# Kernel tuning notes

Measured on AMD Instinct MI355X. Metric: run time of the kernel, lower is better.

Reference implementation:

```python
import jax, jax.numpy as jnp
import numpy as np

N = 50000
HID = 128
NH = 4
E_RES, E_SEQ, E_KNN = 100000, 100000, 200000
BN_EPS = 1e-5
NEG_SLOPE = 0.2


def _gat(h, src, dst, W, al, ar, resW, b):
    """DGL-style GATConv (eval mode: feat_drop off, residual=True, bias).
    h: (N, in), W/resW: (in, H*out), al/ar: (H, out), b: (H*out,)"""
    Hh, out = al.shape
    feat = (h @ W).reshape(N, Hh, out)                 # (N, H, out)
    el = jnp.sum(feat * al, axis=-1)                   # (N, H)
    er = jnp.sum(feat * ar, axis=-1)                   # (N, H)
    e = jax.nn.leaky_relu(el[src] + er[dst], NEG_SLOPE)  # (E, H)
    # edge softmax over incoming edges of each dst node (numerically stable)
    m = jax.ops.segment_max(e, dst, num_segments=N)    # (N, H)
    ex = jnp.exp(e - m[dst])
    s = jax.ops.segment_sum(ex, dst, num_segments=N)
    a = ex / s[dst]                                    # (E, H)
    msg = a[:, :, None] * feat[src]                    # (E, H, out)
    rst = jax.ops.segment_sum(msg, dst, num_segments=N)  # (N, H, out)
    return rst + (h @ resW).reshape(N, Hh, out) + b.reshape(1, Hh, out)


def _hetero(h, src_res, dst_res, src_seq, dst_seq, src_knn, dst_knn, W, al, ar, resW, b):
    # HeteroGraphConv with aggregate='sum' over relations, then mean over heads
    r = _gat(h, src_res, dst_res, W[0], al[0], ar[0], resW[0], b[0])
    r = r + _gat(h, src_seq, dst_seq, W[1], al[1], ar[1], resW[1], b[1])
    r = r + _gat(h, src_knn, dst_knn, W[2], al[2], ar[2], resW[2], b[2])
    return jnp.mean(r, axis=1)                         # (N, out)


def setup_inputs() -> dict:
    key = jax.random.key(0)
    ks = iter(jax.random.split(key, 32))
    inp = {}
    inp["x"] = jax.random.normal(next(ks), (N, HID), jnp.float32)
    inp["src_res"] = jax.random.randint(next(ks), (E_RES,), 0, N, jnp.int32)
    inp["dst_res"] = jax.random.randint(next(ks), (E_RES,), 0, N, jnp.int32)
    inp["src_seq"] = jax.random.randint(next(ks), (E_SEQ,), 0, N, jnp.int32)
    inp["dst_seq"] = jax.random.randint(next(ks), (E_SEQ,), 0, N, jnp.int32)
    inp["src_knn"] = jax.random.randint(next(ks), (E_KNN,), 0, N, jnp.int32)
    inp["dst_knn"] = jax.random.randint(next(ks), (E_KNN,), 0, N, jnp.int32)
    sc = 0.05
    for l in (0, 1):
        inp[f"W{l}"] = jax.random.normal(next(ks), (3, HID, NH * HID), jnp.float32) * sc
        inp[f"al{l}"] = jax.random.normal(next(ks), (3, NH, HID), jnp.float32) * sc
        inp[f"ar{l}"] = jax.random.normal(next(ks), (3, NH, HID), jnp.float32) * sc
        inp[f"resW{l}"] = jax.random.normal(next(ks), (3, HID, NH * HID), jnp.float32) * sc
        inp[f"b{l}"] = jax.random.normal(next(ks), (3, NH * HID), jnp.float32) * sc
    inp["fc_W"] = jax.random.normal(next(ks), (HID, HID), jnp.float32) * sc
    inp["fc_b"] = jax.random.normal(next(ks), (HID,), jnp.float32) * sc
    inp["bn_gamma"] = jnp.ones((HID,), jnp.float32)
    inp["bn_beta"] = jnp.zeros((HID,), jnp.float32)
    inp["bn_mean"] = jax.random.normal(next(ks), (HID,), jnp.float32) * sc
    inp["bn_var"] = jax.random.uniform(next(ks), (HID,), jnp.float32)
    return inp


def reference(x, src_res, dst_res, src_seq, dst_seq, src_knn, dst_knn,
              W0, al0, ar0, resW0, b0, W1, al1, ar1, resW1, b1,
              fc_W, fc_b, bn_gamma, bn_beta, bn_mean, bn_var):
    # layer 0: hetero GAT, head-mean, fc + ReLU + BatchNorm (eval), dropout=identity
    h = _hetero(x, src_res, dst_res, src_seq, dst_seq, src_knn, dst_knn,
                W0, al0, ar0, resW0, b0)
    h = jax.nn.relu(h @ fc_W + fc_b)
    h = (h - bn_mean) / jnp.sqrt(bn_var + BN_EPS) * bn_gamma + bn_beta
    # layer 1 (final): hetero GAT, head-mean
    out = _hetero(h, src_res, dst_res, src_seq, dst_seq, src_knn, dst_knn,
                  W1, al1, ar1, resW1, b1)
    return out
```

## Files before the change

### kernel.cpp

```cpp
#include <hip/hip_runtime.h>
#include <hip/hip_bf16.h>
#include <math.h>
#include <stdint.h>

#define NNODES 50000
#define SCHUNK 4096
#define AW 1664
#define XOFF 1536

typedef __bf16 bf16x8 __attribute__((ext_vector_type(8)));
typedef float f32x4 __attribute__((ext_vector_type(4)));
typedef unsigned short u16;
typedef unsigned int u32;

__device__ __forceinline__ float lrelu(float x){ return x >= 0.f ? x : 0.2f*x; }
__device__ __forceinline__ float b2f(u16 u){ union{ u32 i; float f; } c; c.i = ((u32)u)<<16; return c.f; }
__device__ __forceinline__ float lo2f(u32 v){ union{ u32 i; float f; } c; c.i = v<<16; return c.f; }
__device__ __forceinline__ float hi2f(u32 v){ union{ u32 i; float f; } c; c.i = v & 0xffff0000u; return c.f; }
__device__ __forceinline__ u16 f2b(float f){ __hip_bfloat16 h = __float2bfloat16(f); return *(u16*)&h; }
__device__ __forceinline__ u32 packbf(float a, float b){ return (u32)f2b(a) | ((u32)f2b(b) << 16); }

__global__ void prep_b(const float* __restrict__ W0, const float* __restrict__ W1,
                       const float* __restrict__ resW0, const float* __restrict__ resW1,
                       const float* __restrict__ b0, const float* __restrict__ b1,
                       u16* __restrict__ Btb, float* __restrict__ biasf)
{
    int gid = blockIdx.x*blockDim.x + threadIdx.x;
    if (gid < 2*128*AW){
        int l = gid / (128*AW);
        int rem = gid - l*(128*AW);
        int c = rem / AW;
        int j = rem - c*AW;
        const float* W  = l ? W1 : W0;
        const float* rw = l ? resW1 : resW0;
        float v;
        if (j < XOFF){
            int r = j >> 9, h = (j >> 7) & 3, k = j & 127;
            v = 0.25f * W[(size_t)r*65536 + (size_t)k*512 + h*128 + c];
        } else {
            int k = j - XOFF;
            float s = 0.f;
            for (int r = 0; r < 3; ++r)
                for (int h = 0; h < 4; ++h)
                    s += rw[(size_t)r*65536 + (size_t)k*512 + h*128 + c];
            v = 0.25f * s;
        }
        Btb[gid] = f2b(v);
    }
    if (gid < 256){
        int l = gid >> 7, c = gid & 127;
        const float* bb = l ? b1 : b0;
        float s = 0.f;
        for (int r = 0; r < 3; ++r)
            for (int h = 0; h < 4; ++h)
                s += bb[r*512 + h*128 + c];
        biasf[gid] = 0.25f*s;
    }
}

__global__ void prep_wl(const float* __restrict__ W0, const float* __restrict__ W1,
                        const float* __restrict__ al0, const float* __restrict__ ar0,
                        const float* __restrict__ al1, const float* __restrict__ ar1,
                        const float* __restrict__ fcW,
                        u16* __restrict__ wlb, u16* __restrict__ fcWtb)
{
    int gid = blockIdx.x*blockDim.x + threadIdx.x;
    if (gid < 2*128*128){
        int l = gid >> 14;
        int col = (gid >> 7) & 127;
        int k = gid & 127;
        float v = 0.f;
        if (col < 24){
            int r = col >> 3, lr = (col >> 2) & 1, h = col & 3;
            const float* W = l ? W1 : W0;
            const float* av = l ? (lr ? ar1 : al1) : (lr ? ar0 : al0);
            const float* wrow = W + (size_t)r*65536 + (size_t)k*512 + h*128;
            const float* arow = av + r*512 + h*128;
            for (int cc = 0; cc < 128; ++cc) v += wrow[cc]*arow[cc];
        }
        wlb[gid] = f2b(v);
    }
    if (gid < 128*128){
        int k = gid & 127, n = gid >> 7;
        fcWtb[gid] = f2b(fcW[k*128 + n]);
    }
}

__global__ __launch_bounds__(256) void xprep_kernel(const float* __restrict__ x,
    u16* __restrict__ Ax, const u16* __restrict__ wl, float* __restrict__ el, int M)
{
    __shared__ u16 Xs[64*136];
    __shared__ u16 Ws[32*136];
    const int tid = threadIdx.x;
    const int row0 = blockIdx.x*64;
    #pragma unroll
    for (int p = 0; p < 2; ++p){
        int idx = tid + p*256;
        int c = idx >> 4, kc = (idx & 15)*8;
        float4 v = make_float4(0.f,0.f,0.f,0.f);
        if (c < 24) v = *(const float4*)(wl + c*128 + kc);
        *(float4*)&Ws[c*136 + kc] = v;
    }
    int r = tid >> 2, cq = (tid & 3)*32;
    int grow = row0 + r;
    if (grow < M){
        #pragma unroll
        for (int i = 0; i < 8; ++i){
            float4 v = *(const float4*)(x + (size_t)grow*128 + cq + i*4);
            ushort4 o;
            o.x = f2b(v.x); o.y = f2b(v.y); o.z = f2b(v.z); o.w = f2b(v.w);
            *(ushort4*)(Ax + (size_t)grow*AW + cq + i*4) = o;
            *(ushort4*)&Xs[r*136 + cq + i*4] = o;
        }
    } else {
        ushort4 z; z.x=0; z.y=0; z.z=0; z.w=0;
        #pragma unroll
        for (int i = 0; i < 8; ++i) *(ushort4*)&Xs[r*136 + cq + i*4] = z;
    }
    __syncthreads();
    const int lane = tid & 63, wave = tid >> 6;
    const int r16 = lane & 15, quad = lane >> 4;
    f32x4 acc0 = {}, acc1 = {};
    #pragma unroll
    for (int ks = 0; ks < 4; ++ks){
        int ko = ks*32 + quad*8;
        bf16x8 a  = *(const bf16x8*)&Xs[(wave*16 + r16)*136 + ko];
        bf16x8 b0 = *(const bf16x8*)&Ws[r16*136 + ko];
        bf16x8 b1 = *(const bf16x8*)&Ws[(16 + r16)*136 + ko];
        acc0 = __builtin_amdgcn_mfma_f32_16x16x32_bf16(a, b0, acc0, 0,0,0);
        acc1 = __builtin_amdgcn_mfma_f32_16x16x32_bf16(a, b1, acc1, 0,0,0);
    }
    #pragma unroll
    for (int p = 0; p < 4; ++p){
        int row = row0 + wave*16 + quad*4 + p;
        if (row < M){
            el[(size_t)row*32 + r16] = acc0[p];
            if (r16 < 8) el[(size_t)row*32 + 16 + r16] = acc1[p];
        }
    }
}

__global__ void hist_all(const int* __restrict__ d0, const int* __restrict__ d1,
                         const int* __restrict__ d2, int e0, int e1, int e2,
                         int* __restrict__ cnt)
{
    int g = blockIdx.x*blockDim.x + threadIdx.x;
    if (g >= e0 + e1 + e2) return;
    int rel, idx;
    if (g < e0){ rel = 0; idx = g; }
    else if (g < e0 + e1){ rel = 1; idx = g - e0; }
    else { rel = 2; idx = g - e0 - e1; }
    const int* d = rel == 0 ? d0 : (rel == 1 ? d1 : d2);
    atomicAdd(cnt + (size_t)rel*NNODES + d[idx], 1);
}

__global__ __launch_bounds__(256) void scan_part(const int* __restrict__ cnt_all,
                                                 int* __restrict__ partials, int Nn, int nblk)
{
    int rel = blockIdx.y, blk = blockIdx.x;
    const int* cnt = cnt_all + (size_t)rel*Nn;
    int tid = threadIdx.x;
    int i0 = blk*SCHUNK + tid*16;
    int s = 0;
    #pragma unroll
    for (int k = 0; k < 4; ++k){
        int idx = i0 + k*4;
        if (idx + 3 < Nn){ int4 v = *(const int4*)(cnt + idx); s += v.x+v.y+v.z+v.w; }
        else { for (int j = 0; j < 4; ++j) if (idx+j < Nn) s += cnt[idx+j]; }
    }
    #pragma unroll
    for (int off = 1; off < 64; off <<= 1) s += __shfl_xor(s, off);
    __shared__ int ws[4];
    if ((tid & 63) == 0) ws[tid>>6] = s;
    __syncthreads();
    if (tid == 0) partials[rel*nblk + blk] = ws[0]+ws[1]+ws[2]+ws[3];
}

__global__ __launch_bounds__(256) void scan_write(const int* __restrict__ cnt_all,
                                                  const int* __restrict__ partials,
                                                  int* __restrict__ rp_all, int* __restrict__ cur_all,
                                                  int Nn, int nblk)
{
    int rel = blockIdx.y, blk = blockIdx.x;
    const int* cnt = cnt_all + (size_t)rel*Nn;
    int* rp  = rp_all  + (size_t)rel*(Nn+1);
    int* cur = cur_all + (size_t)rel*Nn;
    int tid = threadIdx.x;
    __shared__ int sOff;
    __shared__ int wsum[4];
    if (tid == 0){
        int o = 0;
        for (int b = 0; b < blk; ++b) o += partials[rel*nblk + b];
        sOff = o;
        if (blk == 0){
            int t = 0;
            for (int b = 0; b < nblk; ++b) t += partials[rel*nblk + b];
            rp[Nn] = t;
        }
    }
    int i0 = blk*SCHUNK + tid*16;
    int v[16];
    int s = 0;
    #pragma unroll
    for (int k = 0; k < 16; ++k){
        int idx = i0 + k;
        v[k] = (idx < Nn) ? cnt[idx] : 0;
        s += v[k];
    }
    int lane = tid & 63;
    int incl = s;
    #pragma unroll
    for (int off = 1; off < 64; off <<= 1){
        int t = __shfl_up(incl, off);
        if (lane >= off) incl += t;
    }
    if (lane == 63) wsum[tid>>6] = incl;
    __syncthreads();
    int woff = 0;
    for (int w = 0; w < (tid>>6); ++w) woff += wsum[w];
    int ex = sOff + woff + incl - s;
    #pragma unroll
    for (int k = 0; k < 16; ++k){
        int idx = i0 + k;
        if (idx < Nn){ rp[idx] = ex; cur[idx] = ex; }
        ex += v[k];
    }
}

__global__ void scatter_all(const int* __restrict__ s0, const int* __restrict__ s1,
                            const int* __restrict__ s2,
                            const int* __restrict__ d0, const int* __restrict__ d1,
                            const int* __restrict__ d2, int e0, int e1, int e2,
                            int* __restrict__ cur, int* __restrict__ colb,
                            int* __restrict__ dste)
{
    int g = blockIdx.x*blockDim.x + threadIdx.x;
    if (g >= e0 + e1 + e2) return;
    int rel, idx, coff;
    if (g < e0){ rel = 0; idx = g; coff = 0; }
    else if (g < e0 + e1){ rel = 1; idx = g - e0; coff = e0; }
    else { rel = 2; idx = g - e0 - e1; coff = e0 + e1; }
    const int* sp = rel == 0 ? s0 : (rel == 1 ? s1 : s2);
    const int* dp = rel == 0 ? d0 : (rel == 1 ? d1 : d2);
    int d = dp[idx];
    int pos = atomicAdd(cur + (size_t)rel*NNODES + d, 1);
    colb[coff + pos] = sp[idx];
    dste[coff + pos] = d;
}

__global__ void wprep(const int* __restrict__ colb, const int* __restrict__ dste,
                      int e0, int e01, int etot,
                      const float* __restrict__ el_all, ushort4* __restrict__ colw)
{
    int j = blockIdx.x*blockDim.x + threadIdx.x;
    if (j >= etot) return;
    int rel = (j < e0) ? 0 : ((j < e01) ? 1 : 2);
    int src = colb[j], dst = dste[j];
    float4 es = *(const float4*)(el_all + (size_t)src*32 + rel*8);
    float4 ed = *(const float4*)(el_all + (size_t)dst*32 + rel*8 + 4);
    ushort4 o;
    o.x = f2b(__expf(lrelu(es.x + ed.x)));
    o.y = f2b(__expf(lrelu(es.y + ed.y)));
    o.z = f2b(__expf(lrelu(es.z + ed.z)));
    o.w = f2b(__expf(lrelu(es.w + ed.w)));
    colw[j] = o;
}

__global__ __launch_bounds__(256) void agg2(const int* __restrict__ rowp_all,
    const int* __restrict__ colb_all, const ushort4* __restrict__ colw_all,
    int e0, int e01,
    const u16* __restrict__ Ax, u16* __restrict__ Abuf, int Nn)
{
    const int rel = blockIdx.y;
    const int tid = threadIdx.x;
    const int lane = tid & 63;
    const int hl = lane & 31;
    const int halfbase = lane & 32;
    const int n = (blockIdx.x*256 + tid) >> 5;
    if (n >= Nn) return;
    const int* rowp = rowp_all + (size_t)rel*(Nn+1);
    const int coff = (rel == 0) ? 0 : ((rel == 1) ? e0 : e01);
    const int* colb = colb_all + coff;
    const ushort4* colw = colw_all + coff;
    u16* op = Abuf + (size_t)n*AW + rel*512 + hl*4;

    int beg = rowp[n], end = rowp[n+1];
    if (beg >= end){
        uint2 z; z.x = 0; z.y = 0;
        #pragma unroll
        for (int h = 0; h < 4; ++h) *(uint2*)(op + h*128) = z;
        return;
    }
    float acc[4][4] = {};
    float us0 = 0.f, us1 = 0.f, us2 = 0.f, us3 = 0.f;
    for (int eb = beg; eb < end; eb += 32){
        int j = eb + hl;
        int s = 0; uint2 w2; w2.x = 0; w2.y = 0;
        if (j < end){
            s = colb[j];
            w2 = *(const uint2*)&colw[j];
        }
        us0 += lo2f(w2.x); us1 += hi2f(w2.x);
        us2 += lo2f(w2.y); us3 += hi2f(w2.y);
        int cnt = min(32, end - eb);
        for (int t = 0; t < cnt; ++t){
            int lsrc = halfbase + t;
            int st = __shfl(s, lsrc);
            u32 wa = (u32)__shfl((int)w2.x, lsrc);
            u32 wb = (u32)__shfl((int)w2.y, lsrc);
            float w0 = lo2f(wa), w1 = hi2f(wa), w2f = lo2f(wb), w3 = hi2f(wb);
            uint2 xv = *(const uint2*)(Ax + (size_t)st*AW + hl*4);
            float x0 = lo2f(xv.x), x1 = hi2f(xv.x), x2 = lo2f(xv.y), x3 = hi2f(xv.y);
            acc[0][0] = fmaf(w0, x0, acc[0][0]); acc[0][1] = fmaf(w0, x1, acc[0][1]);
            acc[0][2] = fmaf(w0, x2, acc[0][2]); acc[0][3] = fmaf(w0, x3, acc[0][3]);
            acc[1][0] = fmaf(w1, x0, acc[1][0]); acc[1][1] = fmaf(w1, x1, acc[1][1]);
            acc[1][2] = fmaf(w1, x2, acc[1][2]); acc[1][3] = fmaf(w1, x3, acc[1][3]);
            acc[2][0] = fmaf(w2f, x0, acc[2][0]); acc[2][1] = fmaf(w2f, x1, acc[2][1]);
            acc[2][2] = fmaf(w2f, x2, acc[2][2]); acc[2][3] = fmaf(w2f, x3, acc[2][3]);
            acc[3][0] = fmaf(w3, x0, acc[3][0]); acc[3][1] = fmaf(w3, x1, acc[3][1]);
            acc[3][2] = fmaf(w3, x2, acc[3][2]); acc[3][3] = fmaf(w3, x3, acc[3][3]);
        }
    }
    #pragma unroll
    for (int off = 1; off < 32; off <<= 1){
        us0 += __shfl_xor(us0, off); us1 += __shfl_xor(us1, off);
        us2 += __shfl_xor(us2, off); us3 += __shfl_xor(us3, off);
    }
    float inv[4] = {1.f/us0, 1.f/us1, 1.f/us2, 1.f/us3};
    #pragma unroll
    for (int h = 0; h < 4; ++h){
        uint2 o;
        o.x = packbf(acc[h][0]*inv[h], acc[h][1]*inv[h]);
        o.y = packbf(acc[h][2]*inv[h], acc[h][3]*inv[h]);
        *(uint2*)(op + h*128) = o;
    }
}

template<int EPI, int ELR>
__global__ __launch_bounds__(256) void gemm_f(
    const u16* __restrict__ A, int Astride, int K,
    const u16* __restrict__ Bt,
    float* __restrict__ Cf, u16* __restrict__ Cb, int Cstride, int M,
    const float* __restrict__ bias, const float* __restrict__ gamma,
    const float* __restrict__ beta, const float* __restrict__ mean,
    const float* __restrict__ var,
    const u16* __restrict__ wl, float* __restrict__ el)
{
    __shared__ u16 smem[13056];
    u16* As = smem;
    u16* Bs = smem + 4096;
    const int tid = threadIdx.x;
    const int row0 = blockIdx.x*64;
    const int lane = tid & 63, wave = tid >> 6;
    const int wm = (wave >> 1)*32, wn = (wave & 1)*64;
    const int r16 = lane & 15, quad = lane >> 4;
    const int swzbase = r16 & 7;
    f32x4 acc[2][4] = {};

    for (int k0 = 0; k0 < K; k0 += 64){
        #pragma unroll
        for (int p = 0; p < 2; ++p){
            int idx = tid + p*256;
            int r = idx >> 3, kc = idx & 7;
            int gr = row0 + r;
            float4 v = make_float4(0.f,0.f,0.f,0.f);
            if (gr < M) v = *(const float4*)(A + (size_t)gr*Astride + k0 + kc*8);
            *(float4*)&As[r*64 + ((kc ^ (r & 7)) << 3)] = v;
        }
        #pragma unroll
        for (int p = 0; p < 4; ++p){
            int idx = tid + p*256;
            int r = idx >> 3, kc = idx & 7;
            float4 v = *(const float4*)(Bt + (size_t)r*K + k0 + kc*8);
            *(float4*)&Bs[r*64 + ((kc ^ (r & 7)) << 3)] = v;
        }
        __syncthreads();
        #pragma unroll
        for (int ks = 0; ks < 2; ++ks){
            int swz = ((ks*4 + quad) ^ swzbase) << 3;
            bf16x8 a0 = *(const bf16x8*)&As[(wm + r16)*64 + swz];
            bf16x8 a1 = *(const bf16x8*)&As[(wm + 16 + r16)*64 + swz];
            #pragma unroll
            for (int j = 0; j < 4; ++j){
                bf16x8 b = *(const bf16x8*)&Bs[(wn + j*16 + r16)*64 + swz];
                acc[0][j] = __builtin_amdgcn_mfma_f32_16x16x32_bf16(a0, b, acc[0][j], 0,0,0);
                acc[1][j] = __builtin_amdgcn_mfma_f32_16x16x32_bf16(a1, b, acc[1][j], 0,0,0);
            }
        }
        __syncthreads();
    }

    u16* Cs = smem;
    u16* Ws = smem + 64*136;
    if (ELR){
        #pragma unroll
        for (int p = 0; p < 2; ++p){
            int idx = tid + p*256;
            int c = idx >> 4, kc = (idx & 15)*8;
            float4 v = make_float4(0.f,0.f,0.f,0.f);
            if (c < 24) v = *(const float4*)(wl + c*128 + kc);
            *(float4*)&Ws[c*136 + kc] = v;
        }
    }
    #pragma unroll
    for (int i = 0; i < 2; ++i){
        #pragma unroll
        for (int p = 0; p < 4; ++p){
            int rl = wm + i*16 + quad*4 + p;
            int row = row0 + rl;
            #pragma unroll
            for (int j = 0; j < 4; ++j){
                int col = wn + j*16 + r16;
                float v = acc[i][j][p] + bias[col];
                if (EPI == 2){
                    float t = fmaxf(v, 0.f);
                    v = (t - mean[col]) * rsqrtf(var[col] + 1e-5f) * gamma[col] + beta[col];
                }
                u16 vb = f2b(v);
                if (row < M){
                    if (EPI == 1) Cf[(size_t)row*Cstride + col] = v;
                    else          Cb[(size_t)row*Cstride + col] = vb;
                }
                if (ELR) Cs[rl*136 + col] = vb;
            }
        }
    }
    if (ELR){
        __syncthreads();
        f32x4 e0 = {}, e1 = {};
        #pragma unroll
        for (int ks = 0; ks < 4; ++ks){
            int ko = ks*32 + quad*8;
            bf16x8 a  = *(const bf16x8*)&Cs[(wave*16 + r16)*136 + ko];
            bf16x8 b0 = *(const bf16x8*)&Ws[r16*136 + ko];
            bf16x8 b1 = *(const bf16x8*)&Ws[(16 + r16)*136 + ko];
            e0 = __builtin_amdgcn_mfma_f32_16x16x32_bf16(a, b0, e0, 0,0,0);
            e1 = __builtin_amdgcn_mfma_f32_16x16x32_bf16(a, b1, e1, 0,0,0);
        }
        #pragma unroll
        for (int p = 0; p < 4; ++p){
            int row = row0 + wave*16 + quad*4 + p;
            if (row < M){
                el[(size_t)row*32 + r16] = e0[p];
                if (r16 < 8) el[(size_t)row*32 + 16 + r16] = e1[p];
            }
        }
    }
}

static inline char* align256(char* p){ return (char*)(((uintptr_t)p + 255) & ~(uintptr_t)255); }

extern "C" void kernel_launch(void* const* d_in, const int* in_sizes, int n_in,
                              void* d_out, int out_size, void* d_ws, size_t ws_size,
                              hipStream_t stream)
{
    const float* x      = (const float*)d_in[0];
    const int* srcs[3]  = {(const int*)d_in[1], (const int*)d_in[3], (const int*)d_in[5]};
    const int* dsts[3]  = {(const int*)d_in[2], (const int*)d_in[4], (const int*)d_in[6]};
    const int  E[3]     = {in_sizes[1], in_sizes[3], in_sizes[5]};
    const float* W0     = (const float*)d_in[7];
    const float* al0    = (const float*)d_in[8];
    const float* ar0    = (const float*)d_in[9];
    const float* resW0  = (const float*)d_in[10];
    const float* b0     = (const float*)d_in[11];
    const float* W1     = (const float*)d_in[12];
    const float* al1    = (const float*)d_in[13];
    const float* ar1    = (const float*)d_in[14];
    const float* resW1  = (const float*)d_in[15];
    const float* b1     = (const float*)d_in[16];
    const float* fcW    = (const float*)d_in[17];
    const float* fcb    = (const float*)d_in[18];
    const float* gamma  = (const float*)d_in[19];
    const float* beta   = (const float*)d_in[20];
    const float* bmean  = (const float*)d_in[21];
    const float* bvar   = (const float*)d_in[22];
    float* out = (float*)d_out;

    char* p = (char*)d_ws;
    u16*   Abuf  = (u16*)p;   p += (size_t)NNODES*AW*2;    p = align256(p);
    float* el    = (float*)p; p += (size_t)NNODES*32*4;    p = align256(p);
    u16*   hmb   = (u16*)p;   p += (size_t)NNODES*128*2;   p = align256(p);
    int*   cnt   = (int*)p;   p += (size_t)3*NNODES*4;     p = align256(p);
    int*   rowp  = (int*)p;   p += (size_t)3*(NNODES+1)*4; p = align256(p);
    int*   cur   = (int*)p;   p += (size_t)3*NNODES*4;     p = align256(p);
    int*   colb  = (int*)p;   p += (size_t)(E[0]+E[1]+E[2])*4; p = align256(p);
    int*   dste  = (int*)p;   p += (size_t)(E[0]+E[1]+E[2])*4; p = align256(p);
    ushort4* colw= (ushort4*)p; p += (size_t)(E[0]+E[1]+E[2])*8; p = align256(p);
    u16*   Btb   = (u16*)p;   p += (size_t)2*128*AW*2;     p = align256(p);
    u16*   wlb   = (u16*)p;   p += (size_t)2*128*128*2;    p = align256(p);
    u16*   fcWtb = (u16*)p;   p += (size_t)128*128*2;      p = align256(p);
    float* biasf = (float*)p; p += (size_t)2*128*4;        p = align256(p);
    int*   parts = (int*)p;   p += (size_t)3*64*4;

    const int NBLK = (NNODES + SCHUNK - 1)/SCHUNK;
    const int MB = (NNODES + 63)/64;
    const int AGGBLKS = (NNODES + 7)/8;
    const int ETOT = E[0] + E[1] + E[2];
    dim3 blk(256);
    u16* Ax = Abuf + XOFF;

    hipMemsetAsync(cnt, 0, (size_t)3*NNODES*sizeof(int), stream);
    prep_b <<<(2*128*AW + 255)/256, blk, 0, stream>>>(W0, W1, resW0, resW1, b0, b1, Btb, biasf);
    prep_wl<<<(2*128*128 + 255)/256, blk, 0, stream>>>(W0, W1, al0, ar0, al1, ar1, fcW, wlb, fcWtb);
    xprep_kernel<<<MB, blk, 0, stream>>>(x, Ax, wlb, el, NNODES);
    hist_all<<<(ETOT + 255)/256, blk, 0, stream>>>(dsts[0], dsts[1], dsts[2], E[0], E[1], E[2], cnt);
    scan_part <<<dim3(NBLK,3), blk, 0, stream>>>(cnt, parts, NNODES, NBLK);
    scan_write<<<dim3(NBLK,3), blk, 0, stream>>>(cnt, parts, rowp, cur, NNODES, NBLK);
    scatter_all<<<(ETOT + 255)/256, blk, 0, stream>>>(srcs[0], srcs[1], srcs[2],
                                                      dsts[0], dsts[1], dsts[2],
                                                      E[0], E[1], E[2], cur, colb, dste);

    wprep<<<(ETOT + 255)/256, blk, 0, stream>>>(colb, dste, E[0], E[0]+E[1], ETOT, el, colw);
    agg2<<<dim3(AGGBLKS,3), blk, 0, stream>>>(rowp, colb, colw, E[0], E[0]+E[1], Ax, Abuf, NNODES);
    gemm_f<4,0><<<MB, blk, 0, stream>>>(Abuf, AW, AW, Btb, nullptr, hmb, 128, NNODES,
                                        biasf, nullptr, nullptr, nullptr, nullptr, nullptr, nullptr);
    gemm_f<2,1><<<MB, blk, 0, stream>>>(hmb, 128, 128, fcWtb, nullptr, Ax, AW, NNODES,
                                        fcb, gamma, beta, bmean, bvar, wlb + 16384, el);

    wprep<<<(ETOT + 255)/256, blk, 0, stream>>>(colb, dste, E[0], E[0]+E[1], ETOT, el, colw);
    agg2<<<dim3(AGGBLKS,3), blk, 0, stream>>>(rowp, colb, colw, E[0], E[0]+E[1], Ax, Abuf, NNODES);
    gemm_f<1,0><<<MB, blk, 0, stream>>>(Abuf, AW, AW, Btb + (size_t)128*AW, out, nullptr, 128, NNODES,
                                        biasf + 128, nullptr, nullptr, nullptr, nullptr, nullptr, nullptr);
}
```

Before: 390.5 us.

## Double-buffer GEMM tiles via direct global-to-LDS loads

The bf16 MFMA GEMM mainloop now loads A and B tiles with global_load_lds 16-byte transfers straight into shared memory, instead of staging them through registers. The XOR swizzle moves from the LDS destination address to the global source offset. Two LDS buffers are used, so the next K-slice is fetched while the current one is multiplied. Shared memory per block grows, which may lower occupancy. Out-of-range A rows are clamped to the last valid row rather than zero-filled.

New measurement: 392.5 us. Within noise of the previous version (+0.5%).

```diff
diff --git a/kernel.cpp b/kernel.cpp
--- a/kernel.cpp
+++ b/kernel.cpp
@@ -19,6 +19,10 @@
 __device__ __forceinline__ float hi2f(u32 v){ union{ u32 i; float f; } c; c.i = v & 0xffff0000u; return c.f; }
 __device__ __forceinline__ u16 f2b(float f){ __hip_bfloat16 h = __float2bfloat16(f); return *(u16*)&h; }
 __device__ __forceinline__ u32 packbf(float a, float b){ return (u32)f2b(a) | ((u32)f2b(b) << 16); }
+
+#define GLDS16(g, l) __builtin_amdgcn_global_load_lds( \
+    (const __attribute__((address_space(1))) void*)(g), \
+    (__attribute__((address_space(3))) void*)(l), 16, 0, 0)
 
 __global__ void prep_b(const float* __restrict__ W0, const float* __restrict__ W1,
                        const float* __restrict__ resW0, const float* __restrict__ resW1,
@@ -346,9 +350,7 @@
     const float* __restrict__ var,
     const u16* __restrict__ wl, float* __restrict__ el)
 {
-    __shared__ u16 smem[13056];
-    u16* As = smem;
-    u16* Bs = smem + 4096;
+    __shared__ u16 smem[24576];
     const int tid = threadIdx.x;
     const int row0 = blockIdx.x*64;
     const int lane = tid & 63, wave = tid >> 6;
@@ -357,24 +359,36 @@
     const int swzbase = r16 & 7;
     f32x4 acc[2][4] = {};
 
-    for (int k0 = 0; k0 < K; k0 += 64){
-        #pragma unroll
-        for (int p = 0; p < 2; ++p){
-            int idx = tid + p*256;
-            int r = idx >> 3, kc = idx & 7;
-            int gr = row0 + r;
-            float4 v = make_float4(0.f,0.f,0.f,0.f);
-            if (gr < M) v = *(const float4*)(A + (size_t)gr*Astride + k0 + kc*8);
-            *(float4*)&As[r*64 + ((kc ^ (r & 7)) << 3)] = v;
-        }
-        #pragma unroll
-        for (int p = 0; p < 4; ++p){
-            int idx = tid + p*256;
-            int r = idx >> 3, kc = idx & 7;
-            float4 v = *(const float4*)(Bt + (size_t)r*K + k0 + kc*8);
-            *(float4*)&Bs[r*64 + ((kc ^ (r & 7)) << 3)] = v;
-        }
-        __syncthreads();
+    const int r8 = lane >> 3, jc = lane & 7;
+    const int soff = ((jc ^ r8) << 3);
+    int gA0 = row0 + wave*16 + r8;      if (gA0 >= M) gA0 = M - 1;
+    int gA1 = row0 + wave*16 + 8 + r8;  if (gA1 >= M) gA1 = M - 1;
+    const u16* srcA0 = A + (size_t)gA0*Astride + soff;
+    const u16* srcA1 = A + (size_t)gA1*Astride + soff;
+    const u16* srcB0 = Bt + (size_t)(wave*32      + r8)*K + soff;
+    const u16* srcB1 = Bt + (size_t)(wave*32 + 8  + r8)*K + soff;
+    const u16* srcB2 = Bt + (size_t)(wave*32 + 16 + r8)*K + soff;
+    const u16* srcB3 = Bt + (size_t)(wave*32 + 24 + r8)*K + soff;
+    const int nk = K >> 6;
+
+    #define STAGE(buf, k0) do { \
+        u16* As_ = smem + (buf)*12288; \
+        u16* Bs_ = As_ + 4096; \
+        GLDS16(srcA0 + (k0), As_ + wave*1024); \
+        GLDS16(srcA1 + (k0), As_ + wave*1024 + 512); \
+        GLDS16(srcB0 + (k0), Bs_ + wave*2048); \
+        GLDS16(srcB1 + (k0), Bs_ + wave*2048 + 512); \
+        GLDS16(srcB2 + (k0), Bs_ + wave*2048 + 1024); \
+        GLDS16(srcB3 + (k0), Bs_ + wave*2048 + 1536); \
+    } while (0)
+
+    STAGE(0, 0);
+    __syncthreads();
+    for (int t = 0; t < nk; ++t){
+        int cur = t & 1;
+        if (t + 1 < nk) STAGE(cur ^ 1, (t + 1) << 6);
+        const u16* As = smem + cur*12288;
+        const u16* Bs = As + 4096;
         #pragma unroll
         for (int ks = 0; ks < 2; ++ks){
             int swz = ((ks*4 + quad) ^ swzbase) << 3;
@@ -389,6 +403,7 @@
         }
         __syncthreads();
     }
+    #undef STAGE
 
     u16* Cs = smem;
     u16* Ws = smem + 64*136;
```
